# Performance work log

Hardware: AMD Instinct MI355X
Metric: run time of the kernel (lower is better)

## Reference

```python
import jax, jax.numpy as jnp
import numpy as np

B, T, D = 4, 1024, 1024
H, HD = 16, 64
DFF = 4096
EPS = 1e-5


def _ln(x, g, b):
    mu = jnp.mean(x, axis=-1, keepdims=True)
    var = jnp.var(x, axis=-1, keepdims=True)
    return (x - mu) * jax.lax.rsqrt(var + EPS) * g + b


def _attn(q_in, kv_in, wq, bq, wk, bk, wv, bv, wo, bo):
    # q_in: [B,Tq,D], kv_in: [B,Tk,D]
    Tq, Tk = q_in.shape[1], kv_in.shape[1]
    q = (q_in @ wq + bq).reshape(B, Tq, H, HD).transpose(0, 2, 1, 3)
    k = (kv_in @ wk + bk).reshape(B, Tk, H, HD).transpose(0, 2, 1, 3)
    v = (kv_in @ wv + bv).reshape(B, Tk, H, HD).transpose(0, 2, 1, 3)
    att = jnp.einsum('bhqd,bhkd->bhqk', q, k) * (1.0 / np.sqrt(HD))
    causal = jnp.tril(jnp.ones((Tq, Tk), dtype=bool))
    att = jnp.where(causal, att, -jnp.inf)
    att = jax.nn.softmax(att, axis=-1)
    y = jnp.einsum('bhqk,bhkd->bhqd', att, v)
    y = y.transpose(0, 2, 1, 3).reshape(B, Tq, H * HD)
    return y @ wo + bo


def setup_inputs() -> dict:
    key = jax.random.key(0)
    ks = jax.random.split(key, 20)
    g = lambda k, shp, scale: (jax.random.normal(k, shp, jnp.float32) * scale)
    s_d = 1.0 / np.sqrt(D)
    s_f = 1.0 / np.sqrt(DFF)
    inp = {
        'x_encoder': jax.random.normal(ks[0], (B, T, D), jnp.float32),
        'x': jax.random.normal(ks[1], (B, T, D), jnp.float32),
        'ln1_g': jnp.ones((D,), jnp.float32), 'ln1_b': jnp.zeros((D,), jnp.float32),
        'ln2_g': jnp.ones((D,), jnp.float32), 'ln2_b': jnp.zeros((D,), jnp.float32),
        'sa_wq': g(ks[2], (D, D), s_d), 'sa_bq': jnp.zeros((D,), jnp.float32),
        'sa_wk': g(ks[3], (D, D), s_d), 'sa_bk': jnp.zeros((D,), jnp.float32),
        'sa_wv': g(ks[4], (D, D), s_d), 'sa_bv': jnp.zeros((D,), jnp.float32),
        'sa_wo': g(ks[5], (D, D), s_d), 'sa_bo': jnp.zeros((D,), jnp.float32),
        'ca_wq': g(ks[6], (D, D), s_d), 'ca_bq': jnp.zeros((D,), jnp.float32),
        'ca_wk': g(ks[7], (D, D), s_d), 'ca_bk': jnp.zeros((D,), jnp.float32),
        'ca_wv': g(ks[8], (D, D), s_d), 'ca_bv': jnp.zeros((D,), jnp.float32),
        'ca_wo': g(ks[9], (D, D), s_d), 'ca_bo': jnp.zeros((D,), jnp.float32),
        'mlp_w1': g(ks[10], (D, DFF), s_d), 'mlp_b1': jnp.zeros((DFF,), jnp.float32),
        'mlp_w2': g(ks[11], (DFF, D), s_f), 'mlp_b2': jnp.zeros((D,), jnp.float32),
    }
    return inp


def reference(x_encoder, x, ln1_g, ln1_b, ln2_g, ln2_b,
              sa_wq, sa_bq, sa_wk, sa_bk, sa_wv, sa_bv, sa_wo, sa_bo,
              ca_wq, ca_bq, ca_wk, ca_bk, ca_wv, ca_bv, ca_wo, ca_bo,
              mlp_w1, mlp_b1, mlp_w2, mlp_b2):
    # x = x + SelfAttn(ln1(x))
    x = x + _attn(_ln(x, ln1_g, ln1_b), _ln(x, ln1_g, ln1_b),
                  sa_wq, sa_bq, sa_wk, sa_bk, sa_wv, sa_bv, sa_wo, sa_bo)
    # x = x + CrossAttn(x_encoder, ln1(x))  (note: ln1 reused, causal mask on dec x enc)
    x = x + _attn(_ln(x, ln1_g, ln1_b), x_encoder,
                  ca_wq, ca_bq, ca_wk, ca_bk, ca_wv, ca_bv, ca_wo, ca_bo)
    # MLP with exact GELU (torch nn.GELU default)
    h = _ln(x, ln2_g, ln2_b)
    h = jax.nn.gelu(h @ mlp_w1 + mlp_b1, approximate=False) @ mlp_w2 + mlp_b2
    return x + h
```

## Files before the change

### kernel.cpp

```cpp
#include <hip/hip_runtime.h>
#include <hip/hip_bf16.h>

typedef __bf16 bf16;
typedef __attribute__((ext_vector_type(4))) __bf16 bf16x4;
typedef __attribute__((ext_vector_type(8))) __bf16 bf16x8;
typedef __attribute__((ext_vector_type(4))) float f32x4;

#define MFMA16(a, b, c) __builtin_amdgcn_mfma_f32_16x16x32_bf16(a, b, c, 0, 0, 0)

#define LGKM_FENCE()                                      \
  do {                                                    \
    asm volatile("s_waitcnt lgkmcnt(0)" ::: "memory");    \
    __builtin_amdgcn_sched_barrier(0);                    \
  } while (0)

#define SCHED0() __builtin_amdgcn_sched_barrier(0)
#define SBAR() __builtin_amdgcn_s_barrier()
#define PRIO(x) __builtin_amdgcn_s_setprio(x)

typedef __attribute__((address_space(1))) void gvoid;
typedef __attribute__((address_space(3))) void lvoid;
__device__ __forceinline__ void gl16(const bf16* g, bf16* l) {
  __builtin_amdgcn_global_load_lds((gvoid*)g, (lvoid*)l, 16, 0, 0);
}


struct PrepArgs {
  const float* wsq[8];
  const float* w1;
  const float* w2;
  const float* xe;
  const float* bs[5];
  bf16* wt8;
  bf16* w1t;
  bf16* w2t;
  bf16* xebf;
  float* bq3;
  float* bkv2;
};

__global__ __launch_bounds__(256) void prep_k(PrepArgs a) {
  __shared__ float t[32][33];
  const int blk = blockIdx.x, tid = threadIdx.x;
  const int tx = tid & 31, ty = tid >> 5;
  if (blk < 8192) {
    const int z = blk >> 10, b = blk & 1023;
    const float* w = a.wsq[z];
    bf16* wt = a.wt8 + ((size_t)z << 20);
    const int nb = (b & 31) * 32, kb = (b >> 5) * 32;
    for (int i = 0; i < 4; ++i)
      t[ty + i * 8][tx] = w[(size_t)(kb + ty + i * 8) * 1024 + nb + tx];
    __syncthreads();
    for (int i = 0; i < 4; ++i)
      wt[(size_t)(nb + ty + i * 8) * 1024 + kb + tx] = (bf16)t[tx][ty + i * 8];
  } else if (blk < 12288) {
    const int b = blk - 8192;
    const int nb = (b & 127) * 32, kb = (b >> 7) * 32;
    for (int i = 0; i < 4; ++i)
      t[ty + i * 8][tx] = a.w1[(size_t)(kb + ty + i * 8) * 4096 + nb + tx];
    __syncthreads();
    for (int i = 0; i < 4; ++i)
      a.w1t[(size_t)(nb + ty + i * 8) * 1024 + kb + tx] = (bf16)t[tx][ty + i * 8];
  } else if (blk < 16384) {
    const int b = blk - 12288;
    const int nb = (b & 31) * 32, kb = (b >> 5) * 32;
    for (int i = 0; i < 4; ++i)
      t[ty + i * 8][tx] = a.w2[(size_t)(kb + ty + i * 8) * 1024 + nb + tx];
    __syncthreads();
    for (int i = 0; i < 4; ++i)
      a.w2t[(size_t)(nb + ty + i * 8) * 4096 + kb + tx] = (bf16)t[tx][ty + i * 8];
  } else if (blk < 20480) {
    const int i = (blk - 16384) * 256 + tid;
    const float4 v = ((const float4*)a.xe)[i];
    bf16* o = a.xebf + (size_t)i * 4;
    o[0] = (bf16)v.x; o[1] = (bf16)v.y; o[2] = (bf16)v.z; o[3] = (bf16)v.w;
  } else {
    const int i = blk - 20480;
    float* d = (i < 3) ? a.bq3 + i * 1024 : a.bkv2 + (i - 3) * 1024;
    ((float4*)d)[tid] = ((const float4*)a.bs[i])[tid];
  }
}

__global__ __launch_bounds__(512) void vtrans_k(const bf16* __restrict__ V0,
                                                const bf16* __restrict__ V1,
                                                bf16* __restrict__ T0,
                                                bf16* __restrict__ T1) {
  const bf16* Vp = blockIdx.z ? V1 : V0;
  bf16* Vt = blockIdx.z ? T1 : T0;
  __shared__ bf16 tl[64][72];
  const int tt = blockIdx.x, bh = blockIdx.y;
  const int b = bh >> 4, h = bh & 15;
  const int tid = threadIdx.x;
  const int row = tid >> 3, ck = tid & 7;
  *(bf16x8*)&tl[row][ck * 8] =
      *(const bf16x8*)&Vp[(size_t)(b * 1024 + tt * 64 + row) * 1024 + h * 64 + ck * 8];
  __syncthreads();
  const int hd = tid >> 3, tc = tid & 7;
  bf16 tmp[8];
#pragma unroll
  for (int e = 0; e < 8; ++e) tmp[e] = tl[tc * 8 + e][hd];
  *(bf16x8*)&Vt[(size_t)(bh * 64 + hd) * 1024 + tt * 64 + tc * 8] = *(bf16x8*)tmp;
}

template <typename TIN>
__global__ __launch_bounds__(256) void ln_k(const TIN* __restrict__ x,
                                            const float* __restrict__ g,
                                            const float* __restrict__ bta,
                                            bf16* __restrict__ out) {
  const int row = blockIdx.x, tid = threadIdx.x;
  float v0, v1, v2, v3;
  if constexpr (sizeof(TIN) == 4) {
    const float4 v = ((const float4*)((const float*)x + (size_t)row * 1024))[tid];
    v0 = v.x; v1 = v.y; v2 = v.z; v3 = v.w;
  } else {
    const bf16x4 v = *(const bf16x4*)((const bf16*)x + (size_t)row * 1024 + tid * 4);
    v0 = (float)v[0]; v1 = (float)v[1]; v2 = (float)v[2]; v3 = (float)v[3];
  }
  float s = v0 + v1 + v2 + v3;
  float sq = v0 * v0 + v1 * v1 + v2 * v2 + v3 * v3;
  for (int d = 1; d < 64; d <<= 1) { s += __shfl_xor(s, d); sq += __shfl_xor(sq, d); }
  __shared__ float rs[4], rq[4];
  const int w = tid >> 6, lane = tid & 63;
  if (lane == 0) { rs[w] = s; rq[w] = sq; }
  __syncthreads();
  s = rs[0] + rs[1] + rs[2] + rs[3];
  sq = rq[0] + rq[1] + rq[2] + rq[3];
  const float mean = s * (1.0f / 1024.0f);
  const float var = sq * (1.0f / 1024.0f) - mean * mean;
  const float rstd = rsqrtf(var + 1e-5f);
  const float4 gv = ((const float4*)g)[tid];
  const float4 bv = ((const float4*)bta)[tid];
  bf16* o = out + (size_t)row * 1024 + tid * 4;
  o[0] = (bf16)((v0 - mean) * rstd * gv.x + bv.x);
  o[1] = (bf16)((v1 - mean) * rstd * gv.y + bv.y);
  o[2] = (bf16)((v2 - mean) * rstd * gv.z + bv.z);
  o[3] = (bf16)((v3 - mean) * rstd * gv.w + bv.w);
}

template <int EPI>
__global__ __launch_bounds__(256) void gemm_k(const bf16* __restrict__ A,
                                              const bf16* __restrict__ Bt,
                                              const float* __restrict__ bias,
                                              void* __restrict__ o0,
                                              int K, int N) {
  __shared__ bf16 As[2][128 * 64];
  __shared__ bf16 Bs[2][128 * 64];
  const int tid = threadIdx.x;
  const int lane = tid & 63, w = tid >> 6;
  const int wr = w >> 1, wc = w & 1;
  const int l15 = lane & 15, l4 = lane >> 4;
  const int gx = gridDim.x;
  const int nwg = gx * gridDim.y;
  const int flat = blockIdx.x + blockIdx.y * gx;
  const int swz = (flat & 7) * (nwg >> 3) + (flat >> 3);
  const size_t bm = swz / gx, bn = swz % gx;
  const bf16* Ab = A + bm * 128 * (size_t)K;
  const bf16* Bb = Bt + bn * 128 * (size_t)K;

  const f32x4 zero4 = {0.f, 0.f, 0.f, 0.f};
  f32x4 acc[4][4];
  for (int m = 0; m < 4; ++m)
    for (int n = 0; n < 4; ++n) acc[m][n] = zero4;

  const int srow = lane >> 3;
  const int gck = ((lane & 7) ^ srow) * 8;
  auto stage = [&](int buf, int t) {
    const int kt = t * 64;
    for (int j = 0; j < 4; ++j) {
      const int row = w * 32 + j * 8 + srow;
      bf16* la = As[buf] + (w * 256 + j * 64 + lane) * 8;
      bf16* lb = Bs[buf] + (w * 256 + j * 64 + lane) * 8;
      gl16(Ab + (size_t)row * K + kt + gck, la);
      gl16(Bb + (size_t)row * K + kt + gck, lb);
    }
  };
  const int xr = l15 & 7;
  const int c0 = (l4 ^ xr) * 8, c1 = ((4 + l4) ^ xr) * 8;
  auto compute = [&](int buf) {
    bf16x8 af[4][2], bfr[4][2];
    for (int m = 0; m < 4; ++m) {
      const int ro = (wr * 64 + m * 16 + l15) * 64;
      af[m][0] = *(const bf16x8*)&As[buf][ro + c0];
      af[m][1] = *(const bf16x8*)&As[buf][ro + c1];
    }
    for (int n = 0; n < 4; ++n) {
      const int ro = (wc * 64 + n * 16 + l15) * 64;
      bfr[n][0] = *(const bf16x8*)&Bs[buf][ro + c0];
      bfr[n][1] = *(const bf16x8*)&Bs[buf][ro + c1];
    }
    PRIO(1);
    for (int m = 0; m < 4; ++m)
      for (int n = 0; n < 4; ++n) {
        acc[m][n] = MFMA16(af[m][0], bfr[n][0], acc[m][n]);
        acc[m][n] = MFMA16(af[m][1], bfr[n][1], acc[m][n]);
      }
    PRIO(0);
  };

  const int nt = K >> 6;
  stage(0, 0);
  stage(1, 1);
  int cur = 0;
  for (int t = 0; t < nt - 2; ++t) {
    asm volatile("s_waitcnt vmcnt(8)" ::: "memory");
    SBAR(); SCHED0();
    compute(cur);
    SCHED0(); SBAR(); SCHED0();
    stage(cur, t + 2);
    cur ^= 1;
  }
  asm volatile("s_waitcnt vmcnt(8)" ::: "memory");
  SBAR(); SCHED0();
  compute(cur);
  cur ^= 1;
  asm volatile("s_waitcnt vmcnt(0)" ::: "memory");
  SBAR(); SCHED0();
  compute(cur);

  for (int m = 0; m < 4; ++m) {
    const int row0 = (int)bm * 128 + wr * 64 + m * 16 + l4 * 4;
    for (int n = 0; n < 4; ++n) {
      const int col = (int)bn * 128 + wc * 64 + n * 16 + l15;
      const float bv = bias[col];
      for (int r = 0; r < 4; ++r) {
        const int row = row0 + r;
        const float v = acc[m][n][r] + bv;
        const float gl = 0.5f * v * (1.0f + erff(v * 0.70710678118f));
        ((bf16*)o0)[(size_t)row * N + col] = (bf16)gl;
      }
    }
  }
}

__global__ __launch_bounds__(256) void gemmqkv_k(const bf16* __restrict__ Aln,
                                                 const bf16* __restrict__ Axe,
                                                 const bf16* __restrict__ wtq,
                                                 const bf16* __restrict__ wtkv,
                                                 const float* __restrict__ bq3,
                                                 const float* __restrict__ bkv2,
                                                 bf16* __restrict__ Qb,
                                                 bf16* __restrict__ Kb1,
                                                 bf16* __restrict__ Vp1,
                                                 bf16* __restrict__ Kb2,
                                                 bf16* __restrict__ Vp2) {
  const int K = 1024;
  __shared__ bf16 As[2][128 * 64];
  __shared__ bf16 Bs[2][128 * 64];
  const int tid = threadIdx.x;
  const int lane = tid & 63, w = tid >> 6;
  const int wr = w >> 1, wc = w & 1;
  const int l15 = lane & 15, l4 = lane >> 4;
  const int gx = 40;
  const int nwg = 40 * 32;
  const int flat = blockIdx.x + blockIdx.y * gx;
  const int swz = (flat & 7) * (nwg >> 3) + (flat >> 3);
  const size_t bm = swz / gx, bn = swz % gx;
  const bool qkv = bn < 24;
  const bf16* Ab = (qkv ? Aln : Axe) + bm * 128 * (size_t)K;
  const bf16* Bb = qkv ? (wtq + bn * 128 * (size_t)K)
                       : (wtkv + (bn - 24) * 128 * (size_t)K);

  const f32x4 zero4 = {0.f, 0.f, 0.f, 0.f};
  f32x4 acc[4][4];
  for (int m = 0; m < 4; ++m)
    for (int n = 0; n < 4; ++n) acc[m][n] = zero4;

  const int srow = lane >> 3;
  const int gck = ((lane & 7) ^ srow) * 8;
  auto stage = [&](int buf, int t) {
    const int kt = t * 64;
    for (int j = 0; j < 4; ++j) {
      const int row = w * 32 + j * 8 + srow;
      bf16* la = As[buf] + (w * 256 + j * 64 + lane) * 8;
      bf16* lb = Bs[buf] + (w * 256 + j * 64 + lane) * 8;
      gl16(Ab + (size_t)row * K + kt + gck, la);
      gl16(Bb + (size_t)row * K + kt + gck, lb);
    }
  };
  const int xr = l15 & 7;
  const int c0 = (l4 ^ xr) * 8, c1 = ((4 + l4) ^ xr) * 8;
  auto compute = [&](int buf) {
    bf16x8 af[4][2], bfr[4][2];
    for (int m = 0; m < 4; ++m) {
      const int ro = (wr * 64 + m * 16 + l15) * 64;
      af[m][0] = *(const bf16x8*)&As[buf][ro + c0];
      af[m][1] = *(const bf16x8*)&As[buf][ro + c1];
    }
    for (int n = 0; n < 4; ++n) {
      const int ro = (wc * 64 + n * 16 + l15) * 64;
      bfr[n][0] = *(const bf16x8*)&Bs[buf][ro + c0];
      bfr[n][1] = *(const bf16x8*)&Bs[buf][ro + c1];
    }
    PRIO(1);
    for (int m = 0; m < 4; ++m)
      for (int n = 0; n < 4; ++n) {
        acc[m][n] = MFMA16(af[m][0], bfr[n][0], acc[m][n]);
        acc[m][n] = MFMA16(af[m][1], bfr[n][1], acc[m][n]);
      }
    PRIO(0);
  };

  const int nt = K >> 6;
  stage(0, 0);
  stage(1, 1);
  int cur = 0;
  for (int t = 0; t < nt - 2; ++t) {
    asm volatile("s_waitcnt vmcnt(8)" ::: "memory");
    SBAR(); SCHED0();
    compute(cur);
    SCHED0(); SBAR(); SCHED0();
    stage(cur, t + 2);
    cur ^= 1;
  }
  asm volatile("s_waitcnt vmcnt(8)" ::: "memory");
  SBAR(); SCHED0();
  compute(cur);
  cur ^= 1;
  asm volatile("s_waitcnt vmcnt(0)" ::: "memory");
  SBAR(); SCHED0();
  compute(cur);

  for (int m = 0; m < 4; ++m) {
    const int row0 = (int)bm * 128 + wr * 64 + m * 16 + l4 * 4;
    for (int n = 0; n < 4; ++n) {
      const int coln = (qkv ? (int)bn : (int)bn - 24) * 128 + wc * 64 + n * 16 + l15;
      const float bv = qkv ? bq3[coln] : bkv2[coln];
      const int which = coln >> 10, c = coln & 1023;
      bf16* op = qkv ? (which == 0 ? Qb : (which == 1 ? Kb1 : Vp1))
                     : (which == 0 ? Kb2 : Vp2);
      for (int r = 0; r < 4; ++r) {
        const int row = row0 + r;
        op[(size_t)row * 1024 + c] = (bf16)(acc[m][n][r] + bv);
      }
    }
  }
}

template <int EPI>
__global__ __launch_bounds__(256) void gemm64_k(const bf16* __restrict__ A,
                                                const bf16* __restrict__ Bt,
                                                const float* __restrict__ bias,
                                                const void* __restrict__ res,
                                                void* __restrict__ o0,
                                                int K, int N) {
  __shared__ bf16 As[2][128 * 64];
  __shared__ bf16 Bs[2][64 * 64];
  const int tid = threadIdx.x;
  const int lane = tid & 63, w = tid >> 6;
  const int l15 = lane & 15, l4 = lane >> 4;
  const int gx = gridDim.x;
  const int nwg = gx * gridDim.y;
  const int flat = blockIdx.x + blockIdx.y * gx;
  const int swz = (flat & 7) * (nwg >> 3) + (flat >> 3);
  const size_t bm = swz / gx, bn = swz % gx;
  const bf16* Ab = A + bm * 128 * (size_t)K;
  const bf16* Bb = Bt + bn * 64 * (size_t)K;

  const f32x4 zero4 = {0.f, 0.f, 0.f, 0.f};
  f32x4 acc[2][4];
  for (int m = 0; m < 2; ++m)
    for (int n = 0; n < 4; ++n) acc[m][n] = zero4;

  const int srow = lane >> 3;
  const int gck = ((lane & 7) ^ srow) * 8;
  auto stage = [&](int buf, int t) {
    const int kt = t * 64;
    for (int j = 0; j < 4; ++j) {
      const int row = w * 32 + j * 8 + srow;
      gl16(Ab + (size_t)row * K + kt + gck, As[buf] + (w * 256 + j * 64 + lane) * 8);
    }
    for (int j = 0; j < 2; ++j) {
      const int row = w * 16 + j * 8 + srow;
      gl16(Bb + (size_t)row * K + kt + gck, Bs[buf] + (w * 128 + j * 64 + lane) * 8);
    }
  };
  const int xr = l15 & 7;
  const int c0 = (l4 ^ xr) * 8, c1 = ((4 + l4) ^ xr) * 8;
  auto compute = [&](int buf) {
    bf16x8 af[2][2], bfr[4][2];
    for (int m = 0; m < 2; ++m) {
      const int ro = (w * 32 + m * 16 + l15) * 64;
      af[m][0] = *(const bf16x8*)&As[buf][ro + c0];
      af[m][1] = *(const bf16x8*)&As[buf][ro + c1];
    }
    for (int n = 0; n < 4; ++n) {
      const int ro = (n * 16 + l15) * 64;
      bfr[n][0] = *(const bf16x8*)&Bs[buf][ro + c0];
      bfr[n][1] = *(const bf16x8*)&Bs[buf][ro + c1];
    }
    PRIO(1);
    for (int m = 0; m < 2; ++m)
      for (int n = 0; n < 4; ++n) {
        acc[m][n] = MFMA16(af[m][0], bfr[n][0], acc[m][n]);
        acc[m][n] = MFMA16(af[m][1], bfr[n][1], acc[m][n]);
      }
    PRIO(0);
  };

  const int nt = K >> 6;
  stage(0, 0);
  stage(1, 1);
  int cur = 0;
  for (int t = 0; t < nt - 2; ++t) {
    asm volatile("s_waitcnt vmcnt(6)" ::: "memory");
    SBAR(); SCHED0();
    compute(cur);
    SCHED0(); SBAR(); SCHED0();
    stage(cur, t + 2);
    cur ^= 1;
  }
  asm volatile("s_waitcnt vmcnt(6)" ::: "memory");
  SBAR(); SCHED0();
  compute(cur);
  cur ^= 1;
  asm volatile("s_waitcnt vmcnt(0)" ::: "memory");
  SBAR(); SCHED0();
  compute(cur);

  for (int m = 0; m < 2; ++m) {
    const int row0 = (int)bm * 128 + w * 32 + m * 16 + l4 * 4;
    for (int n = 0; n < 4; ++n) {
      const int col = (int)bn * 64 + n * 16 + l15;
      const float bv = bias[col];
      for (int r = 0; r < 4; ++r) {
        const int row = row0 + r;
        const size_t idx = (size_t)row * N + col;
        float v = acc[m][n][r] + bv;
        if constexpr (EPI == 0) {
          ((bf16*)o0)[idx] = (bf16)v;
        } else if constexpr (EPI == 2) {
          v += ((const float*)res)[idx];
          ((bf16*)o0)[idx] = (bf16)v;
        } else if constexpr (EPI == 4) {
          v += (float)((const bf16*)res)[idx];
          ((bf16*)o0)[idx] = (bf16)v;
        } else {
          v += (float)((const bf16*)res)[idx];
          ((float*)o0)[idx] = v;
        }
      }
    }
  }
}

__global__ __launch_bounds__(512) void attn_k(const bf16* __restrict__ Q,
                                              const bf16* __restrict__ Kb,
                                              const bf16* __restrict__ Vt,
                                              bf16* __restrict__ O) {
  __shared__ bf16 Ks[2][64 * 64];
  __shared__ bf16 Vs[2][64 * 64];
  __shared__ bf16 Plds[8][16][72];
  const int bx = blockIdx.x, bh = blockIdx.y;
  const int b = bh >> 4, h = bh & 15;
  const int tid = threadIdx.x, lane = tid & 63, w = tid >> 6;
  const int myqt = (w < 4) ? bx : (15 - bx);
  const int qbase = myqt * 64 + (w & 3) * 16;
  const int l15 = lane & 15, l4 = lane >> 4;
  const int nt = 16 - bx;

  const bf16* Qp = Q + (size_t)(b * 1024 + qbase + l15) * 1024 + h * 64 + l4 * 8;
  bf16x8 qf0 = *(const bf16x8*)Qp;
  bf16x8 qf1 = *(const bf16x8*)(Qp + 32);
  for (int i = 0; i < 8; ++i) {
    qf0[i] = (bf16)((float)qf0[i] * 0.125f);
    qf1[i] = (bf16)((float)qf1[i] * 0.125f);
  }
  bf16x8 onesf;
  for (int i = 0; i < 8; ++i) onesf[i] = (bf16)1.0f;

  const f32x4 zero4 = {0.f, 0.f, 0.f, 0.f};
  f32x4 o[4], ol;
  float mrow[4];
  for (int d = 0; d < 4; ++d) o[d] = zero4;
  ol = zero4;
  for (int r = 0; r < 4; ++r) mrow[r] = -1e30f;

  const int qrow0 = qbase + l4 * 4;

  const int srow = tid >> 3;
  const int cg = (tid & 7) ^ (srow & 7);
  const bf16* Kg = Kb + (size_t)(b * 1024 + srow) * 1024 + h * 64 + cg * 8;
  const bf16* Vg = Vt + (size_t)(bh * 64 + srow) * 1024 + cg * 8;
  auto stage = [&](int buf, int t) {
    gl16(Kg + (size_t)t * 64 * 1024, Ks[buf] + tid * 8);
    gl16(Vg + t * 64, Vs[buf] + tid * 8);
  };

  const int xr = l15 & 7;
  const int fc0 = (l4 ^ xr) * 8, fc1 = ((4 + l4) ^ xr) * 8;

  auto compute = [&](int buf, int kt) {
    const int kbase = kt * 64;
    f32x4 s[4];
    for (int n = 0; n < 4; ++n) s[n] = zero4;
    PRIO(1);
    for (int n = 0; n < 4; ++n) {
      const int ro = (n * 16 + l15) * 64;
      const bf16x8 kf0 = *(const bf16x8*)&Ks[buf][ro + fc0];
      const bf16x8 kf1 = *(const bf16x8*)&Ks[buf][ro + fc1];
      s[n] = MFMA16(qf0, kf0, s[n]);
      s[n] = MFMA16(qf1, kf1, s[n]);
    }
    PRIO(0);
    if (kt == myqt) {
      for (int n = 0; n < 4; ++n) {
        const int kc = kbase + n * 16 + l15;
        for (int r = 0; r < 4; ++r)
          if (kc > qrow0 + r) s[n][r] = -1e30f;
      }
    }
    float mx[4];
    for (int r = 0; r < 4; ++r)
      mx[r] = fmaxf(fmaxf(s[0][r], s[1][r]), fmaxf(s[2][r], s[3][r]));
    for (int d0 = 1; d0 < 16; d0 <<= 1)
      for (int r = 0; r < 4; ++r) mx[r] = fmaxf(mx[r], __shfl_xor(mx[r], d0));
    float alpha[4];
    for (int r = 0; r < 4; ++r) {
      const float mnew = fmaxf(mrow[r], mx[r]);
      alpha[r] = __expf(mrow[r] - mnew);
      mrow[r] = mnew;
    }
    for (int n = 0; n < 4; ++n)
      for (int r = 0; r < 4; ++r) s[n][r] = __expf(s[n][r] - mrow[r]);
    for (int d = 0; d < 4; ++d)
      for (int r = 0; r < 4; ++r) o[d][r] *= alpha[r];
    for (int r = 0; r < 4; ++r) ol[r] *= alpha[r];

    LGKM_FENCE();
    for (int r = 0; r < 4; ++r)
      for (int n = 0; n < 4; ++n)
        Plds[w][l4 * 4 + r][n * 16 + l15] = (bf16)s[n][r];
    LGKM_FENCE();
    const bf16x8 pf0 = *(const bf16x8*)&Plds[w][l15][l4 * 8];
    const bf16x8 pf1 = *(const bf16x8*)&Plds[w][l15][32 + l4 * 8];

    PRIO(1);
    for (int d = 0; d < 4; ++d) {
      const int ro = (d * 16 + l15) * 64;
      const bf16x8 vf0 = *(const bf16x8*)&Vs[buf][ro + fc0];
      const bf16x8 vf1 = *(const bf16x8*)&Vs[buf][ro + fc1];
      o[d] = MFMA16(pf0, vf0, o[d]);
      o[d] = MFMA16(pf1, vf1, o[d]);
    }
    ol = MFMA16(pf0, onesf, ol);
    ol = MFMA16(pf1, onesf, ol);
    PRIO(0);
  };

  stage(0, 0);
  stage(1, 1);
  int cur = 0;
  for (int t = 0; t < nt - 2; ++t) {
    asm volatile("s_waitcnt vmcnt(2)" ::: "memory");
    SBAR(); SCHED0();
    if (t <= myqt) compute(cur, t);
    SCHED0(); SBAR(); SCHED0();
    stage(cur, t + 2);
    cur ^= 1;
  }
  asm volatile("s_waitcnt vmcnt(2)" ::: "memory");
  SBAR(); SCHED0();
  if (nt - 2 <= myqt) compute(cur, nt - 2);
  cur ^= 1;
  asm volatile("s_waitcnt vmcnt(0)" ::: "memory");
  SBAR(); SCHED0();
  if (nt - 1 <= myqt) compute(cur, nt - 1);

  for (int r = 0; r < 4; ++r) {
    const float inv = 1.0f / ol[r];
    for (int d = 0; d < 4; ++d) {
      O[(size_t)(b * 1024 + qbase + l4 * 4 + r) * 1024 + h * 64 + d * 16 + l15] =
          (bf16)(o[d][r] * inv);
    }
  }
}

extern "C" void kernel_launch(void* const* d_in, const int* in_sizes, int n_in,
                              void* d_out, int out_size, void* d_ws, size_t ws_size,
                              hipStream_t stream) {
  const float* x_enc = (const float*)d_in[0];
  const float* x     = (const float*)d_in[1];
  const float* ln1_g = (const float*)d_in[2];
  const float* ln1_b = (const float*)d_in[3];
  const float* ln2_g = (const float*)d_in[4];
  const float* ln2_b = (const float*)d_in[5];
  const float* sa_wq = (const float*)d_in[6];  const float* sa_bq = (const float*)d_in[7];
  const float* sa_wk = (const float*)d_in[8];  const float* sa_bk = (const float*)d_in[9];
  const float* sa_wv = (const float*)d_in[10]; const float* sa_bv = (const float*)d_in[11];
  const float* sa_wo = (const float*)d_in[12]; const float* sa_bo = (const float*)d_in[13];
  const float* ca_wq = (const float*)d_in[14]; const float* ca_bq = (const float*)d_in[15];
  const float* ca_wk = (const float*)d_in[16]; const float* ca_bk = (const float*)d_in[17];
  const float* ca_wv = (const float*)d_in[18]; const float* ca_bv = (const float*)d_in[19];
  const float* ca_wo = (const float*)d_in[20]; const float* ca_bo = (const float*)d_in[21];
  const float* mlp_w1 = (const float*)d_in[22]; const float* mlp_b1 = (const float*)d_in[23];
  const float* mlp_w2 = (const float*)d_in[24]; const float* mlp_b2 = (const float*)d_in[25];

  char* ws = (char*)d_ws;
  size_t off = 0;
  auto take = [&](size_t bytes) { char* p = ws + off; off += (bytes + 255) & ~(size_t)255; return p; };

  bf16* wt8 = (bf16*)take((size_t)8 * 1024 * 1024 * 2);
  bf16* w1t   = (bf16*)take((size_t)4096 * 1024 * 2);
  bf16* w2t   = (bf16*)take((size_t)1024 * 4096 * 2);
  bf16* lnbuf = (bf16*)take((size_t)4096 * 1024 * 2);
  bf16* xe_bf = (bf16*)take((size_t)4096 * 1024 * 2);
  bf16* Qb    = (bf16*)take((size_t)4096 * 1024 * 2);
  bf16* Kb1   = (bf16*)take((size_t)4096 * 1024 * 2);
  bf16* Vp1   = (bf16*)take((size_t)4096 * 1024 * 2);
  bf16* Vt1   = (bf16*)take((size_t)4096 * 1024 * 2);
  bf16* Kb2   = (bf16*)take((size_t)4096 * 1024 * 2);
  bf16* Vp2   = (bf16*)take((size_t)4096 * 1024 * 2);
  bf16* Vt2   = (bf16*)take((size_t)4096 * 1024 * 2);
  bf16* AOb   = (bf16*)take((size_t)4096 * 1024 * 2);
  bf16* x1    = (bf16*)take((size_t)4096 * 1024 * 2);
  bf16* x2    = (bf16*)take((size_t)4096 * 1024 * 2);
  bf16* Hb    = (bf16*)take((size_t)4096 * 4096 * 2);
  float* bq3  = (float*)take((size_t)3072 * 4);
  float* bkv2 = (float*)take((size_t)2048 * 4);

  bf16* wt[8];
  for (int i = 0; i < 8; ++i) wt[i] = wt8 + (size_t)i * 1024 * 1024;

  const dim3 blk(256);
  PrepArgs pa;
  pa.wsq[0] = sa_wq; pa.wsq[1] = sa_wk; pa.wsq[2] = sa_wv; pa.wsq[3] = sa_wo;
  pa.wsq[4] = ca_wq; pa.wsq[5] = ca_wk; pa.wsq[6] = ca_wv; pa.wsq[7] = ca_wo;
  pa.w1 = mlp_w1; pa.w2 = mlp_w2; pa.xe = x_enc;
  pa.bs[0] = sa_bq; pa.bs[1] = sa_bk; pa.bs[2] = sa_bv;
  pa.bs[3] = ca_bk; pa.bs[4] = ca_bv;
  pa.wt8 = wt8; pa.w1t = w1t; pa.w2t = w2t; pa.xebf = xe_bf;
  pa.bq3 = bq3; pa.bkv2 = bkv2;
  prep_k<<<20485, blk, 0, stream>>>(pa);

  ln_k<float><<<4096, blk, 0, stream>>>(x, ln1_g, ln1_b, lnbuf);
  gemmqkv_k<<<dim3(40, 32), blk, 0, stream>>>(lnbuf, xe_bf, wt[0], wt[5],
                                              bq3, bkv2, Qb, Kb1, Vp1, Kb2, Vp2);
  vtrans_k<<<dim3(16, 64, 2), dim3(512), 0, stream>>>(Vp1, Vp2, Vt1, Vt2);

  attn_k<<<dim3(8, 64), dim3(512), 0, stream>>>(Qb, Kb1, Vt1, AOb);
  gemm64_k<2><<<dim3(16, 32), blk, 0, stream>>>(AOb, wt[3], sa_bo, x, x1, 1024, 1024);

  ln_k<bf16><<<4096, blk, 0, stream>>>(x1, ln1_g, ln1_b, lnbuf);
  gemm64_k<0><<<dim3(16, 32), blk, 0, stream>>>(lnbuf, wt[4], ca_bq, nullptr, Qb, 1024, 1024);
  attn_k<<<dim3(8, 64), dim3(512), 0, stream>>>(Qb, Kb2, Vt2, AOb);
  gemm64_k<4><<<dim3(16, 32), blk, 0, stream>>>(AOb, wt[7], ca_bo, x1, x2, 1024, 1024);

  ln_k<bf16><<<4096, blk, 0, stream>>>(x2, ln2_g, ln2_b, lnbuf);
  gemm_k<3><<<dim3(32, 32), blk, 0, stream>>>(lnbuf, w1t, mlp_b1, Hb, 1024, 4096);
  gemm64_k<5><<<dim3(16, 32), blk, 0, stream>>>(Hb, w2t, mlp_b2, x2,
                                                (float*)d_out, 4096, 1024);

  (void)in_sizes; (void)n_in; (void)out_size; (void)ws_size;
}
```

Baseline: 332.7 us.

## Use eight waves per GEMM workgroup, halving per-wave output tiles

```diff
diff --git a/kernel.cpp b/kernel.cpp
--- a/kernel.cpp
+++ b/kernel.cpp
@@ -138,7 +138,7 @@
 }
 
 template <int EPI>
-__global__ __launch_bounds__(256) void gemm_k(const bf16* __restrict__ A,
+__global__ __launch_bounds__(512) void gemm_k(const bf16* __restrict__ A,
                                               const bf16* __restrict__ Bt,
                                               const float* __restrict__ bias,
                                               void* __restrict__ o0,
@@ -158,28 +158,27 @@
   const bf16* Bb = Bt + bn * 128 * (size_t)K;
 
   const f32x4 zero4 = {0.f, 0.f, 0.f, 0.f};
-  f32x4 acc[4][4];
-  for (int m = 0; m < 4; ++m)
+  f32x4 acc[2][4];
+  for (int m = 0; m < 2; ++m)
     for (int n = 0; n < 4; ++n) acc[m][n] = zero4;
 
-  const int srow = lane >> 3;
-  const int gck = ((lane & 7) ^ srow) * 8;
+  const int srow = tid >> 3;
+  const int gck = ((tid & 7) ^ (srow & 7)) * 8;
   auto stage = [&](int buf, int t) {
     const int kt = t * 64;
-    for (int j = 0; j < 4; ++j) {
-      const int row = w * 32 + j * 8 + srow;
-      bf16* la = As[buf] + (w * 256 + j * 64 + lane) * 8;
-      bf16* lb = Bs[buf] + (w * 256 + j * 64 + lane) * 8;
-      gl16(Ab + (size_t)row * K + kt + gck, la);
-      gl16(Bb + (size_t)row * K + kt + gck, lb);
-    }
+    bf16* la = As[buf] + tid * 8;
+    bf16* lb = Bs[buf] + tid * 8;
+    gl16(Ab + (size_t)srow * K + kt + gck, la);
+    gl16(Ab + (size_t)(srow + 64) * K + kt + gck, la + 4096);
+    gl16(Bb + (size_t)srow * K + kt + gck, lb);
+    gl16(Bb + (size_t)(srow + 64) * K + kt + gck, lb + 4096);
   };
   const int xr = l15 & 7;
   const int c0 = (l4 ^ xr) * 8, c1 = ((4 + l4) ^ xr) * 8;
   auto compute = [&](int buf) {
-    bf16x8 af[4][2], bfr[4][2];
-    for (int m = 0; m < 4; ++m) {
-      const int ro = (wr * 64 + m * 16 + l15) * 64;
+    bf16x8 af[2][2], bfr[4][2];
+    for (int m = 0; m < 2; ++m) {
+      const int ro = (wr * 32 + m * 16 + l15) * 64;
       af[m][0] = *(const bf16x8*)&As[buf][ro + c0];
       af[m][1] = *(const bf16x8*)&As[buf][ro + c1];
     }
@@ -189,7 +188,7 @@
       bfr[n][1] = *(const bf16x8*)&Bs[buf][ro + c1];
     }
     PRIO(1);
-    for (int m = 0; m < 4; ++m)
+    for (int m = 0; m < 2; ++m)
       for (int n = 0; n < 4; ++n) {
         acc[m][n] = MFMA16(af[m][0], bfr[n][0], acc[m][n]);
         acc[m][n] = MFMA16(af[m][1], bfr[n][1], acc[m][n]);
@@ -202,14 +201,14 @@
   stage(1, 1);
   int cur = 0;
   for (int t = 0; t < nt - 2; ++t) {
-    asm volatile("s_waitcnt vmcnt(8)" ::: "memory");
+    asm volatile("s_waitcnt vmcnt(4)" ::: "memory");
     SBAR(); SCHED0();
     compute(cur);
     SCHED0(); SBAR(); SCHED0();
     stage(cur, t + 2);
     cur ^= 1;
   }
-  asm volatile("s_waitcnt vmcnt(8)" ::: "memory");
+  asm volatile("s_waitcnt vmcnt(4)" ::: "memory");
   SBAR(); SCHED0();
   compute(cur);
   cur ^= 1;
@@ -217,8 +216,8 @@
   SBAR(); SCHED0();
   compute(cur);
 
-  for (int m = 0; m < 4; ++m) {
-    const int row0 = (int)bm * 128 + wr * 64 + m * 16 + l4 * 4;
+  for (int m = 0; m < 2; ++m) {
+    const int row0 = (int)bm * 128 + wr * 32 + m * 16 + l4 * 4;
     for (int n = 0; n < 4; ++n) {
       const int col = (int)bn * 128 + wc * 64 + n * 16 + l15;
       const float bv = bias[col];
@@ -232,7 +231,7 @@
   }
 }
 
-__global__ __launch_bounds__(256) void gemmqkv_k(const bf16* __restrict__ Aln,
+__global__ __launch_bounds__(512) void gemmqkv_k(const bf16* __restrict__ Aln,
                                                  const bf16* __restrict__ Axe,
                                                  const bf16* __restrict__ wtq,
                                                  const bf16* __restrict__ wtkv,
@@ -261,28 +260,27 @@
                        : (wtkv + (bn - 24) * 128 * (size_t)K);
 
   const f32x4 zero4 = {0.f, 0.f, 0.f, 0.f};
-  f32x4 acc[4][4];
-  for (int m = 0; m < 4; ++m)
+  f32x4 acc[2][4];
+  for (int m = 0; m < 2; ++m)
     for (int n = 0; n < 4; ++n) acc[m][n] = zero4;
 
-  const int srow = lane >> 3;
-  const int gck = ((lane & 7) ^ srow) * 8;
+  const int srow = tid >> 3;
+  const int gck = ((tid & 7) ^ (srow & 7)) * 8;
   auto stage = [&](int buf, int t) {
     const int kt = t * 64;
-    for (int j = 0; j < 4; ++j) {
-      const int row = w * 32 + j * 8 + srow;
-      bf16* la = As[buf] + (w * 256 + j * 64 + lane) * 8;
-      bf16* lb = Bs[buf] + (w * 256 + j * 64 + lane) * 8;
-      gl16(Ab + (size_t)row * K + kt + gck, la);
-      gl16(Bb + (size_t)row * K + kt + gck, lb);
-    }
+    bf16* la = As[buf] + tid * 8;
+    bf16* lb = Bs[buf] + tid * 8;
+    gl16(Ab + (size_t)srow * K + kt + gck, la);
+    gl16(Ab + (size_t)(srow + 64) * K + kt + gck, la + 4096);
+    gl16(Bb + (size_t)srow * K + kt + gck, lb);
+    gl16(Bb + (size_t)(srow + 64) * K + kt + gck, lb + 4096);
   };
   const int xr = l15 & 7;
   const int c0 = (l4 ^ xr) * 8, c1 = ((4 + l4) ^ xr) * 8;
   auto compute = [&](int buf) {
-    bf16x8 af[4][2], bfr[4][2];
-    for (int m = 0; m < 4; ++m) {
-      const int ro = (wr * 64 + m * 16 + l15) * 64;
+    bf16x8 af[2][2], bfr[4][2];
+    for (int m = 0; m < 2; ++m) {
+      const int ro = (wr * 32 + m * 16 + l15) * 64;
       af[m][0] = *(const bf16x8*)&As[buf][ro + c0];
       af[m][1] = *(const bf16x8*)&As[buf][ro + c1];
     }
@@ -292,7 +290,7 @@
       bfr[n][1] = *(const bf16x8*)&Bs[buf][ro + c1];
     }
     PRIO(1);
-    for (int m = 0; m < 4; ++m)
+    for (int m = 0; m < 2; ++m)
       for (int n = 0; n < 4; ++n) {
         acc[m][n] = MFMA16(af[m][0], bfr[n][0], acc[m][n]);
         acc[m][n] = MFMA16(af[m][1], bfr[n][1], acc[m][n]);
@@ -305,14 +303,14 @@
   stage(1, 1);
   int cur = 0;
   for (int t = 0; t < nt - 2; ++t) {
-    asm volatile("s_waitcnt vmcnt(8)" ::: "memory");
+    asm volatile("s_waitcnt vmcnt(4)" ::: "memory");
     SBAR(); SCHED0();
     compute(cur);
     SCHED0(); SBAR(); SCHED0();
     stage(cur, t + 2);
     cur ^= 1;
   }
-  asm volatile("s_waitcnt vmcnt(8)" ::: "memory");
+  asm volatile("s_waitcnt vmcnt(4)" ::: "memory");
   SBAR(); SCHED0();
   compute(cur);
   cur ^= 1;
@@ -320,8 +318,8 @@
   SBAR(); SCHED0();
   compute(cur);
 
-  for (int m = 0; m < 4; ++m) {
-    const int row0 = (int)bm * 128 + wr * 64 + m * 16 + l4 * 4;
+  for (int m = 0; m < 2; ++m) {
+    const int row0 = (int)bm * 128 + wr * 32 + m * 16 + l4 * 4;
     for (int n = 0; n < 4; ++n) {
       const int coln = (qkv ? (int)bn : (int)bn - 24) * 128 + wc * 64 + n * 16 + l15;
       const float bv = qkv ? bq3[coln] : bkv2[coln];
@@ -337,7 +335,7 @@
 }
 
 template <int EPI>
-__global__ __launch_bounds__(256) void gemm64_k(const bf16* __restrict__ A,
+__global__ __launch_bounds__(512) void gemm64_k(const bf16* __restrict__ A,
                                                 const bf16* __restrict__ Bt,
                                                 const float* __restrict__ bias,
                                                 const void* __restrict__ res,
@@ -357,31 +355,26 @@
   const bf16* Bb = Bt + bn * 64 * (size_t)K;
 
   const f32x4 zero4 = {0.f, 0.f, 0.f, 0.f};
-  f32x4 acc[2][4];
-  for (int m = 0; m < 2; ++m)
-    for (int n = 0; n < 4; ++n) acc[m][n] = zero4;
-
-  const int srow = lane >> 3;
-  const int gck = ((lane & 7) ^ srow) * 8;
+  f32x4 acc[4];
+  for (int n = 0; n < 4; ++n) acc[n] = zero4;
+
+  const int srow = tid >> 3;
+  const int gck = ((tid & 7) ^ (srow & 7)) * 8;
   auto stage = [&](int buf, int t) {
     const int kt = t * 64;
-    for (int j = 0; j < 4; ++j) {
-      const int row = w * 32 + j * 8 + srow;
-      gl16(Ab + (size_t)row * K + kt + gck, As[buf] + (w * 256 + j * 64 + lane) * 8);
-    }
-    for (int j = 0; j < 2; ++j) {
-      const int row = w * 16 + j * 8 + srow;
-      gl16(Bb + (size_t)row * K + kt + gck, Bs[buf] + (w * 128 + j * 64 + lane) * 8);
-    }
+    bf16* la = As[buf] + tid * 8;
+    gl16(Ab + (size_t)srow * K + kt + gck, la);
+    gl16(Ab + (size_t)(srow + 64) * K + kt + gck, la + 4096);
+    gl16(Bb + (size_t)srow * K + kt + gck, Bs[buf] + tid * 8);
   };
   const int xr = l15 & 7;
   const int c0 = (l4 ^ xr) * 8, c1 = ((4 + l4) ^ xr) * 8;
   auto compute = [&](int buf) {
-    bf16x8 af[2][2], bfr[4][2];
-    for (int m = 0; m < 2; ++m) {
-      const int ro = (w * 32 + m * 16 + l15) * 64;
-      af[m][0] = *(const bf16x8*)&As[buf][ro + c0];
-      af[m][1] = *(const bf16x8*)&As[buf][ro + c1];
+    bf16x8 af[2], bfr[4][2];
+    {
+      const int ro = (w * 16 + l15) * 64;
+      af[0] = *(const bf16x8*)&As[buf][ro + c0];
+      af[1] = *(const bf16x8*)&As[buf][ro + c1];
     }
     for (int n = 0; n < 4; ++n) {
       const int ro = (n * 16 + l15) * 64;
@@ -389,11 +382,10 @@
       bfr[n][1] = *(const bf16x8*)&Bs[buf][ro + c1];
     }
     PRIO(1);
-    for (int m = 0; m < 2; ++m)
-      for (int n = 0; n < 4; ++n) {
-        acc[m][n] = MFMA16(af[m][0], bfr[n][0], acc[m][n]);
-        acc[m][n] = MFMA16(af[m][1], bfr[n][1], acc[m][n]);
-      }
+    for (int n = 0; n < 4; ++n) {
+      acc[n] = MFMA16(af[0], bfr[n][0], acc[n]);
+      acc[n] = MFMA16(af[1], bfr[n][1], acc[n]);
+    }
     PRIO(0);
   };
 
@@ -402,14 +394,14 @@
   stage(1, 1);
   int cur = 0;
   for (int t = 0; t < nt - 2; ++t) {
-    asm volatile("s_waitcnt vmcnt(6)" ::: "memory");
+    asm volatile("s_waitcnt vmcnt(3)" ::: "memory");
     SBAR(); SCHED0();
     compute(cur);
     SCHED0(); SBAR(); SCHED0();
     stage(cur, t + 2);
     cur ^= 1;
   }
-  asm volatile("s_waitcnt vmcnt(6)" ::: "memory");
+  asm volatile("s_waitcnt vmcnt(3)" ::: "memory");
   SBAR(); SCHED0();
   compute(cur);
   cur ^= 1;
@@ -417,27 +409,25 @@
   SBAR(); SCHED0();
   compute(cur);
 
-  for (int m = 0; m < 2; ++m) {
-    const int row0 = (int)bm * 128 + w * 32 + m * 16 + l4 * 4;
-    for (int n = 0; n < 4; ++n) {
-      const int col = (int)bn * 64 + n * 16 + l15;
-      const float bv = bias[col];
-      for (int r = 0; r < 4; ++r) {
-        const int row = row0 + r;
-        const size_t idx = (size_t)row * N + col;
-        float v = acc[m][n][r] + bv;
-        if constexpr (EPI == 0) {
-          ((bf16*)o0)[idx] = (bf16)v;
-        } else if constexpr (EPI == 2) {
-          v += ((const float*)res)[idx];
-          ((bf16*)o0)[idx] = (bf16)v;
-        } else if constexpr (EPI == 4) {
-          v += (float)((const bf16*)res)[idx];
-          ((bf16*)o0)[idx] = (bf16)v;
-        } else {
-          v += (float)((const bf16*)res)[idx];
-          ((float*)o0)[idx] = v;
-        }
+  const int row0 = (int)bm * 128 + w * 16 + l4 * 4;
+  for (int n = 0; n < 4; ++n) {
+    const int col = (int)bn * 64 + n * 16 + l15;
+    const float bv = bias[col];
+    for (int r = 0; r < 4; ++r) {
+      const int row = row0 + r;
+      const size_t idx = (size_t)row * N + col;
+      float v = acc[n][r] + bv;
+      if constexpr (EPI == 0) {
+        ((bf16*)o0)[idx] = (bf16)v;
+      } else if constexpr (EPI == 2) {
+        v += ((const float*)res)[idx];
+        ((bf16*)o0)[idx] = (bf16)v;
+      } else if constexpr (EPI == 4) {
+        v += (float)((const bf16*)res)[idx];
+        ((bf16*)o0)[idx] = (bf16)v;
+      } else {
+        v += (float)((const bf16*)res)[idx];
+        ((float*)o0)[idx] = v;
       }
     }
   }
@@ -633,22 +623,22 @@
   prep_k<<<20485, blk, 0, stream>>>(pa);
 
   ln_k<float><<<4096, blk, 0, stream>>>(x, ln1_g, ln1_b, lnbuf);
-  gemmqkv_k<<<dim3(40, 32), blk, 0, stream>>>(lnbuf, xe_bf, wt[0], wt[5],
-                                              bq3, bkv2, Qb, Kb1, Vp1, Kb2, Vp2);
+  gemmqkv_k<<<dim3(40, 32), dim3(512), 0, stream>>>(lnbuf, xe_bf, wt[0], wt[5],
+                                                    bq3, bkv2, Qb, Kb1, Vp1, Kb2, Vp2);
   vtrans_k<<<dim3(16, 64, 2), dim3(512), 0, stream>>>(Vp1, Vp2, Vt1, Vt2);
 
   attn_k<<<dim3(8, 64), dim3(512), 0, stream>>>(Qb, Kb1, Vt1, AOb);
-  gemm64_k<2><<<dim3(16, 32), blk, 0, stream>>>(AOb, wt[3], sa_bo, x, x1, 1024, 1024);
+  gemm64_k<2><<<dim3(16, 32), dim3(512), 0, stream>>>(AOb, wt[3], sa_bo, x, x1, 1024, 1024);
 
   ln_k<bf16><<<4096, blk, 0, stream>>>(x1, ln1_g, ln1_b, lnbuf);
-  gemm64_k<0><<<dim3(16, 32), blk, 0, stream>>>(lnbuf, wt[4], ca_bq, nullptr, Qb, 1024, 1024);
+  gemm64_k<0><<<dim3(16, 32), dim3(512), 0, stream>>>(lnbuf, wt[4], ca_bq, nullptr, Qb, 1024, 1024);
   attn_k<<<dim3(8, 64), dim3(512), 0, stream>>>(Qb, Kb2, Vt2, AOb);
-  gemm64_k<4><<<dim3(16, 32), blk, 0, stream>>>(AOb, wt[7], ca_bo, x1, x2, 1024, 1024);
+  gemm64_k<4><<<dim3(16, 32), dim3(512), 0, stream>>>(AOb, wt[7], ca_bo, x1, x2, 1024, 1024);
 
   ln_k<bf16><<<4096, blk, 0, stream>>>(x2, ln2_g, ln2_b, lnbuf);
-  gemm_k<3><<<dim3(32, 32), blk, 0, stream>>>(lnbuf, w1t, mlp_b1, Hb, 1024, 4096);
-  gemm64_k<5><<<dim3(16, 32), blk, 0, stream>>>(Hb, w2t, mlp_b2, x2,
-                                                (float*)d_out, 4096, 1024);
+  gemm_k<3><<<dim3(32, 32), dim3(512), 0, stream>>>(lnbuf, w1t, mlp_b1, Hb, 1024, 4096);
+  gemm64_k<5><<<dim3(16, 32), dim3(512), 0, stream>>>(Hb, w2t, mlp_b2, x2,
+                                                      (float*)d_out, 4096, 1024);
 
   (void)in_sizes; (void)n_in; (void)out_size; (void)ws_size;
 }
```

New measurement: 316.0 us, median of 2. 5.0% less time.
